# Kernel tuning notes

Measured on AMD Instinct MI355X. Metric: run time of the kernel, lower is better.

Reference implementation:

```python
import jax, jax.numpy as jnp
import numpy as np

B, I, H = 8192, 1024, 1024


def _linear_params(key, out_dim, in_dim):
    kw, kb = jax.random.split(key)
    bound = 1.0 / np.sqrt(in_dim)
    w = jax.random.uniform(kw, (out_dim, in_dim), jnp.float32, -bound, bound)
    b = jax.random.uniform(kb, (out_dim,), jnp.float32, -bound, bound)
    return w, b


def setup_inputs() -> dict:
    key = jax.random.key(0)
    ks = jax.random.split(key, 11)
    x = jax.random.normal(ks[0], (B, I), jnp.float32)
    h = jax.random.normal(ks[1], (B, H), jnp.float32)
    c = jax.random.normal(ks[2], (B, H), jnp.float32)
    # 4 gates: forget(f), input-mask(i), input-candidate(g, tanh), output(o)
    wf_i, bf_i = _linear_params(ks[3], H, I)
    wf_h, bf_h = _linear_params(ks[4], H, H)
    wi_i, bi_i = _linear_params(ks[5], H, I)
    wi_h, bi_h = _linear_params(ks[6], H, H)
    wg_i, bg_i = _linear_params(ks[7], H, I)
    wg_h, bg_h = _linear_params(ks[8], H, H)
    wo_i, bo_i = _linear_params(ks[9], H, I)
    wo_h, bo_h = _linear_params(ks[10], H, H)
    return dict(x=x, h=h, c=c,
                wf_i=wf_i, bf_i=bf_i, wf_h=wf_h, bf_h=bf_h,
                wi_i=wi_i, bi_i=bi_i, wi_h=wi_h, bi_h=bi_h,
                wg_i=wg_i, bg_i=bg_i, wg_h=wg_h, bg_h=bg_h,
                wo_i=wo_i, bo_i=bo_i, wo_h=wo_h, bo_h=bo_h)


def _gate(x, h, w_i, b_i, w_h, b_h, nonlin):
    # Linear(x) + Linear(h) then nonlinearity, matching torch nn.Linear (x @ W.T + b)
    pre = jnp.dot(x, w_i.T) + b_i + jnp.dot(h, w_h.T) + b_h
    return nonlin(pre)


def reference(x, h, c,
              wf_i, bf_i, wf_h, bf_h,
              wi_i, bi_i, wi_h, bi_h,
              wg_i, bg_i, wg_h, bg_h,
              wo_i, bo_i, wo_h, bo_h):
    ft = _gate(x, h, wf_i, bf_i, wf_h, bf_h, jax.nn.sigmoid)
    it = _gate(x, h, wi_i, bi_i, wi_h, bi_h, jax.nn.sigmoid)
    gt = _gate(x, h, wg_i, bg_i, wg_h, bg_h, jnp.tanh)
    ct = ft * c + it * gt
    ot = _gate(x, h, wo_i, bo_i, wo_h, bo_h, jax.nn.sigmoid)
    ht = ot * jnp.tanh(ct)
    return (ht, ct)
```

## Files before the change

kernel.cpp:

```cpp
#include <hip/hip_runtime.h>
#include <hip/hip_bf16.h>

typedef __hip_bfloat16 bf16;
typedef __attribute__((ext_vector_type(8))) short bf16x8;
typedef __attribute__((ext_vector_type(4))) float f32x4;

#define AS1 __attribute__((address_space(1)))
#define AS3 __attribute__((address_space(3)))

__device__ __forceinline__ void async16(const void* g, void* l) {
  __builtin_amdgcn_global_load_lds((const AS1 void*)g, (AS3 void*)l, 16, 0, 0);
}

__device__ __forceinline__ float fsigmoid(float x) { return 1.0f / (1.0f + __expf(-x)); }
__device__ __forceinline__ float ftanh(float x)    { return 1.0f - 2.0f / (__expf(2.0f * x) + 1.0f); }

__device__ __forceinline__ bf16x8 pack8(float4 lo, float4 hi) {
  union { bf16x8 v; unsigned int u[4]; } r;
  r.u[0] = (__float_as_uint(lo.y) & 0xFFFF0000u) | (__float_as_uint(lo.x) >> 16);
  r.u[1] = (__float_as_uint(lo.w) & 0xFFFF0000u) | (__float_as_uint(lo.z) >> 16);
  r.u[2] = (__float_as_uint(hi.y) & 0xFFFF0000u) | (__float_as_uint(hi.x) >> 16);
  r.u[3] = (__float_as_uint(hi.w) & 0xFFFF0000u) | (__float_as_uint(hi.z) >> 16);
  return r.v;
}

__global__ __launch_bounds__(256) void prep_bf16(
    const float* __restrict__ x, const float* __restrict__ h,
    const float* __restrict__ wfi, const float* __restrict__ wii,
    const float* __restrict__ wgi, const float* __restrict__ woi,
    const float* __restrict__ wfh, const float* __restrict__ wih,
    const float* __restrict__ wgh, const float* __restrict__ woh,
    bf16* __restrict__ dst)
{
  const int NC = 3 * 1024 * 1024;
  for (int ci = blockIdx.x * 256 + threadIdx.x; ci < NC; ci += gridDim.x * 256) {
    const float* src; size_t soff, doff;
    if (ci < (1 << 20)) {
      int m = ci >> 7, k = (ci & 127) << 3;
      src = x; soff = (size_t)m * 1024 + k; doff = (size_t)m * 2048 + k;
    } else if (ci < (2 << 20)) {
      int c2 = ci - (1 << 20);
      int m = c2 >> 7, k = (c2 & 127) << 3;
      src = h; soff = (size_t)m * 1024 + k; doff = (size_t)m * 2048 + 1024 + k;
    } else {
      int we  = ci - (2 << 20);
      int mat = we >> 17;
      int wl  = we & ((1 << 17) - 1);
      int hh  = wl >> 7, k = (wl & 127) << 3;
      int g   = mat & 3;
      src = (mat == 0) ? wfi : (mat == 1) ? wii : (mat == 2) ? wgi : (mat == 3) ? woi
          : (mat == 4) ? wfh : (mat == 5) ? wih : (mat == 6) ? wgh : woh;
      soff = (size_t)hh * 1024 + k;
      doff = (size_t)8192 * 2048
           + (size_t)(((hh >> 6) << 8) + (g << 6) + (hh & 63)) * 2048
           + ((mat >> 2) << 10) + k;
    }
    float4 lo = *(const float4*)(src + soff);
    float4 hi = *(const float4*)(src + soff + 4);
    *(bf16x8*)(dst + doff) = pack8(lo, hi);
  }
}

#define VMCNT(N) do { asm volatile("s_waitcnt vmcnt(" #N ")" ::: "memory"); \
                      __builtin_amdgcn_sched_barrier(0); } while (0)

#define PH(t_, kh_, mh_, STAGE_STMT, VMW)                                     \
  {                                                                           \
    const char* Ab = smem + (((t_) & 1) << 16) + ((kh_) << 14);               \
    const char* Bb = Ab + 32768;                                              \
    if ((mh_) == 0) {                                                         \
      _Pragma("unroll") for (int n = 0; n < 4; ++n)                           \
        bfr[n] = *(const bf16x8*)(Bb + boff + (n << 10));                     \
    }                                                                         \
    bf16x8 afr[4];                                                            \
    _Pragma("unroll") for (int i = 0; i < 4; ++i)                             \
      afr[i] = *(const bf16x8*)(Ab + aoff + ((((mh_) << 2) + i) << 10));      \
    STAGE_STMT;                                                               \
    __builtin_amdgcn_s_barrier();                                             \
    __builtin_amdgcn_s_setprio(1);                                            \
    _Pragma("unroll") for (int i = 0; i < 4; ++i)                             \
      _Pragma("unroll") for (int n = 0; n < 4; ++n)                           \
        acc[((mh_) << 2) + i][n] = __builtin_amdgcn_mfma_f32_16x16x32_bf16(   \
            afr[i], bfr[n], acc[((mh_) << 2) + i][n], 0, 0, 0);               \
    __builtin_amdgcn_s_setprio(0);                                            \
    VMW;                                                                      \
    __builtin_amdgcn_s_barrier();                                             \
  }

__global__ __launch_bounds__(512, 2) void lstm_mfma(
    const bf16* __restrict__ ws,
    const float* __restrict__ c,
    const float* __restrict__ bfi, const float* __restrict__ bfh,
    const float* __restrict__ bii, const float* __restrict__ bih,
    const float* __restrict__ bgi, const float* __restrict__ bgh,
    const float* __restrict__ boi, const float* __restrict__ boh,
    float* __restrict__ out)
{
  __shared__ __align__(16) char smem[135168];

  const int tid  = threadIdx.x;
  const int lane = tid & 63;
  const int w    = tid >> 6;
  const int wr   = w >> 2;
  const int wc   = w & 3;
  const int l15  = lane & 15;
  const int quad = lane >> 4;

  const int orig = blockIdx.x;
  const int xcd  = orig & 7;
  const int li   = orig >> 3;
  const int by   = ((xcd >> 1) << 3) + (li & 7);
  const int bx   = ((xcd & 1) << 3) + (li >> 3);
  const int bg0  = by << 8;

  const bf16* Ag = ws + (size_t)bg0 * 2048;
  const bf16* Bg = ws + (size_t)8192 * 2048 + (size_t)(bx << 8) * 2048;

  const int r2 = lane >> 2;
  const int sl = lane & 3;
  const int schunk = ((sl ^ ((r2 >> 1) & 3)) << 3);

  const int slotA = ((quad ^ ((l15 >> 1) & 3)) << 4);
  const int aoff  = ((wr << 7) + l15) * 64 + slotA;
  const int boff  = ((wc << 6) + l15) * 64 + slotA;

  f32x4 acc[8][4];
#pragma unroll
  for (int i = 0; i < 8; ++i)
#pragma unroll
    for (int j = 0; j < 4; ++j) acc[i][j] = (f32x4){0.f, 0.f, 0.f, 0.f};

  auto stageA = [&](int t_, int kh_) {
    const bf16* s = Ag + (size_t)(t_ << 6) + (kh_ << 5) + schunk;
    char* d = smem + ((t_ & 1) << 16) + (kh_ << 14) + (w << 10);
#pragma unroll
    for (int r = 0; r < 2; ++r)
      async16(s + ((size_t)((((r << 3) + w) << 4) + r2)) * 2048, d + (r << 13));
  };
  auto stageB = [&](int t_, int kh_) {
    const bf16* s = Bg + (size_t)(t_ << 6) + (kh_ << 5) + schunk;
    char* d = smem + ((t_ & 1) << 16) + 32768 + (kh_ << 14) + (w << 10);
#pragma unroll
    for (int r = 0; r < 2; ++r)
      async16(s + ((size_t)((((r << 3) + w) << 4) + r2)) * 2048, d + (r << 13));
  };

  stageA(0, 0); stageB(0, 0); stageA(0, 1); stageB(0, 1); stageA(1, 0); stageB(1, 0);
  VMCNT(8);
  __builtin_amdgcn_s_barrier();

  for (int t = 0; t < 30; ++t) {
    bf16x8 bfr[4];
    PH(t, 0, 0, { stageA(t + 1, 1); }, )
    PH(t, 0, 1, { stageB(t + 1, 1); }, VMCNT(8))
    PH(t, 1, 0, { stageA(t + 2, 0); }, )
    PH(t, 1, 1, { stageB(t + 2, 0); }, VMCNT(8))
  }
  {
    const int t = 30;
    bf16x8 bfr[4];
    PH(t, 0, 0, { stageA(31, 1); }, )
    PH(t, 0, 1, { stageB(31, 1); }, VMCNT(8))
    PH(t, 1, 0, , )
    PH(t, 1, 1, , VMCNT(4))
  }
  {
    const int t = 31;
    bf16x8 bfr[4];
    PH(t, 0, 0, , )
    PH(t, 0, 1, , VMCNT(0))
    PH(t, 1, 0, , )
    PH(t, 1, 1, , )
  }

  float* Act = (float*)smem;
  const float* bI = (wc == 0) ? bfi : (wc == 1) ? bii : (wc == 2) ? bgi : boi;
  const float* bH = (wc == 0) ? bfh : (wc == 1) ? bih : (wc == 2) ? bgh : boh;
  const int hcol0 = bx << 6;
  float biasv[4];
#pragma unroll
  for (int n = 0; n < 4; ++n)
    biasv[n] = bI[hcol0 + n * 16 + l15] + bH[hcol0 + n * 16 + l15];

  const size_t outCT = (size_t)8192 * 1024;
  const bool istanh = (wc == 2);

#pragma unroll
  for (int p = 0; p < 2; ++p) {
    __syncthreads();
    if (wr == p) {
      float* Aw = Act + wc * 8448;
#pragma unroll
      for (int m = 0; m < 8; ++m)
#pragma unroll
        for (int n = 0; n < 4; ++n)
#pragma unroll
          for (int r = 0; r < 4; ++r) {
            const float v = acc[m][n][r] + biasv[n];
            Aw[(m * 16 + quad * 4 + r) * 66 + n * 16 + l15] = istanh ? ftanh(v) : fsigmoid(v);
          }
    }
    __syncthreads();
#pragma unroll
    for (int it = 0; it < 16; ++it) {
      const int idx = it * 512 + tid;
      const int row = idx >> 6, col = idx & 63;
      const float fv = Act[row * 66 + col];
      const float iv = Act[8448 + row * 66 + col];
      const float gv = Act[16896 + row * 66 + col];
      const float ov = Act[25344 + row * 66 + col];
      const size_t gi = (size_t)(bg0 + p * 128 + row) * 1024 + hcol0 + col;
      const float ctv = fv * c[gi] + iv * gv;
      const float htv = ov * ftanh(ctv);
      out[gi]         = htv;
      out[outCT + gi] = ctv;
    }
  }
}

__global__ __launch_bounds__(256) void lstm_fused(
    const float* __restrict__ x, const float* __restrict__ h, const float* __restrict__ c,
    const float* __restrict__ wfi, const float* __restrict__ bfi, const float* __restrict__ wfh, const float* __restrict__ bfh,
    const float* __restrict__ wii, const float* __restrict__ bii, const float* __restrict__ wih, const float* __restrict__ bih,
    const float* __restrict__ wgi, const float* __restrict__ bgi, const float* __restrict__ wgh, const float* __restrict__ bgh,
    const float* __restrict__ woi, const float* __restrict__ boi, const float* __restrict__ woh, const float* __restrict__ boh,
    float* __restrict__ out)
{
  __shared__ __align__(16) char smem[33792];
  short* As = (short*)smem;
  short* Bs = As + 8192;
  float* Epi = (float*)smem;

  const int tid  = threadIdx.x;
  const int lane = tid & 63;
  const int w    = tid >> 6;
  const int l15  = lane & 15;
  const int quad = lane >> 4;
  const int rq   = w >> 1;
  const int cq   = w & 1;
  const int rowoff = lane >> 3;
  const int ch   = lane & 7;
  const int dstch = ch ^ rowoff;

  const int bg0 = blockIdx.y << 7;
  const int hb  = blockIdx.x << 5;

  const float* WgI = (w == 0) ? wfi : (w == 1) ? wii : (w == 2) ? wgi : woi;
  const float* WgH = (w == 0) ? wfh : (w == 1) ? wih : (w == 2) ? wgh : woh;

  size_t aoff[4], boff2[4];
#pragma unroll
  for (int q = 0; q < 4; ++q) {
    const int u = (w << 2) + q;
    aoff[q]  = (size_t)((u << 3) + rowoff) * 1024 + (ch << 3);
    boff2[q] = (size_t)((q << 3) + rowoff) * 1024 + (ch << 3);
  }

  f32x4 acc[4][4];
#pragma unroll
  for (int i = 0; i < 4; ++i)
#pragma unroll
    for (int j = 0; j < 4; ++j) acc[i][j] = (f32x4){0.f, 0.f, 0.f, 0.f};

  const int arow = (rq * 64 + l15) * 64;
  const int brow = (cq * 64 + l15) * 64;
  const int sw   = l15 & 7;
  const int c0   = ((0 + quad) ^ sw) << 3;
  const int c1   = ((4 + quad) ^ sw) << 3;

  float4 A0[4], A1[4], B0[4], B1[4];
  auto issue = [&](int KT) {
    const float* Ab = ((KT < 16) ? x : h)     + (size_t)bg0 * 1024 + ((KT & 15) << 6);
    const float* Bb = ((KT < 16) ? WgI : WgH) + (size_t)hb  * 1024 + ((KT & 15) << 6);
#pragma unroll
    for (int q = 0; q < 4; ++q) {
      const float* pa = Ab + aoff[q];
      const float* pb = Bb + boff2[q];
      A0[q] = *(const float4*)pa; A1[q] = *(const float4*)(pa + 4);
      B0[q] = *(const float4*)pb; B1[q] = *(const float4*)(pb + 4);
    }
  };

  issue(0);
  for (int kt = 0; kt < 32; ++kt) {
    __syncthreads();
#pragma unroll
    for (int q = 0; q < 4; ++q) {
      const int u = (w << 2) + q;
      *(bf16x8*)(As + (u * 8 + rowoff) * 64 + (dstch << 3)) = pack8(A0[q], A1[q]);
      *(bf16x8*)(Bs + (u * 8 + rowoff) * 64 + (dstch << 3)) = pack8(B0[q], B1[q]);
    }
    __syncthreads();
    if (kt < 31) issue(kt + 1);

#pragma unroll
    for (int s = 0; s < 2; ++s) {
      const int cs = s ? c1 : c0;
      bf16x8 a[4], b[4];
#pragma unroll
      for (int i = 0; i < 4; ++i) a[i] = *(const bf16x8*)(As + arow + i * 1024 + cs);
#pragma unroll
      for (int j = 0; j < 4; ++j) b[j] = *(const bf16x8*)(Bs + brow + j * 1024 + cs);
#pragma unroll
      for (int i = 0; i < 4; ++i)
#pragma unroll
        for (int j = 0; j < 4; ++j)
          acc[i][j] = __builtin_amdgcn_mfma_f32_16x16x32_bf16(a[i], b[j], acc[i][j], 0, 0, 0);
    }
  }

  const float* bAi = cq ? bgi : bfi;
  const float* bAh = cq ? bgh : bfh;
  const float* bBi = cq ? boi : bii;
  const float* bBh = cq ? boh : bih;
  float biasv[4];
  biasv[0] = bAi[hb + l15]      + bAh[hb + l15];
  biasv[1] = bAi[hb + 16 + l15] + bAh[hb + 16 + l15];
  biasv[2] = bBi[hb + l15]      + bBh[hb + l15];
  biasv[3] = bBi[hb + 16 + l15] + bBh[hb + 16 + l15];

  const size_t outCT = (size_t)8192 * 1024;

#pragma unroll
  for (int p = 0; p < 2; ++p) {
    __syncthreads();
    if (rq == p) {
#pragma unroll
      for (int j = 0; j < 4; ++j) {
        const int  n  = cq * 64 + j * 16 + l15;
        const bool ut = (cq == 1) && (j < 2);
        const float bj = biasv[j];
#pragma unroll
        for (int i = 0; i < 4; ++i)
#pragma unroll
          for (int r = 0; r < 4; ++r) {
            const float v = acc[i][j][r] + bj;
            Epi[(i * 16 + quad * 4 + r) * 132 + n] = ut ? ftanh(v) : fsigmoid(v);
          }
      }
    }
    __syncthreads();
#pragma unroll
    for (int it = 0; it < 8; ++it) {
      const int pair = it * 256 + tid;
      const int row  = pair >> 5;
      const int hl   = pair & 31;
      const float fv = Epi[row * 132 + hl];
      const float iv = Epi[row * 132 + 32 + hl];
      const float gv = Epi[row * 132 + 64 + hl];
      const float ov = Epi[row * 132 + 96 + hl];
      const size_t idx = (size_t)(bg0 + p * 64 + row) * 1024 + hb + hl;
      const float ctv = fv * c[idx] + iv * gv;
      const float htv = ov * ftanh(ctv);
      out[idx]         = htv;
      out[outCT + idx] = ctv;
    }
  }
}

extern "C" void kernel_launch(void* const* d_in, const int* in_sizes, int n_in,
                              void* d_out, int out_size, void* d_ws, size_t ws_size,
                              hipStream_t stream) {
  const float* p[19];
  for (int i = 0; i < 19; ++i) p[i] = (const float*)d_in[i];
  const size_t need = (size_t)24 * 1024 * 1024 * sizeof(bf16);
  if (ws_size >= need) {
    prep_bf16<<<dim3(2048), dim3(256), 0, stream>>>(
        p[0], p[1],
        p[3], p[7], p[11], p[15],
        p[5], p[9], p[13], p[17],
        (bf16*)d_ws);
    lstm_mfma<<<dim3(512), dim3(512), 0, stream>>>(
        (const bf16*)d_ws, p[2],
        p[4], p[6], p[8], p[10], p[12], p[14], p[16], p[18],
        (float*)d_out);
  } else {
    lstm_fused<<<dim3(32, 64), dim3(256), 0, stream>>>(
        p[0], p[1], p[2],
        p[3], p[4], p[5], p[6],
        p[7], p[8], p[9], p[10],
        p[11], p[12], p[13], p[14],
        p[15], p[16], p[17], p[18],
        (float*)d_out);
  }
}
```

Baseline: 349.9 us.

## Software-pipeline LDS fragment reads one phase ahead of MFMA compute

```diff
diff --git a/kernel.cpp b/kernel.cpp
--- a/kernel.cpp
+++ b/kernel.cpp
@@ -64,28 +64,28 @@
 #define VMCNT(N) do { asm volatile("s_waitcnt vmcnt(" #N ")" ::: "memory"); \
                       __builtin_amdgcn_sched_barrier(0); } while (0)
 
-#define PH(t_, kh_, mh_, STAGE_STMT, VMW)                                     \
-  {                                                                           \
-    const char* Ab = smem + (((t_) & 1) << 16) + ((kh_) << 14);               \
-    const char* Bb = Ab + 32768;                                              \
-    if ((mh_) == 0) {                                                         \
-      _Pragma("unroll") for (int n = 0; n < 4; ++n)                           \
-        bfr[n] = *(const bf16x8*)(Bb + boff + (n << 10));                     \
-    }                                                                         \
-    bf16x8 afr[4];                                                            \
-    _Pragma("unroll") for (int i = 0; i < 4; ++i)                             \
-      afr[i] = *(const bf16x8*)(Ab + aoff + ((((mh_) << 2) + i) << 10));      \
-    STAGE_STMT;                                                               \
-    __builtin_amdgcn_s_barrier();                                             \
+#define BAR __builtin_amdgcn_s_barrier()
+
+#define RD_A(dst, t_, kh_, mh_) do {                                          \
+    const char* Ab_ = smem + (((t_) & 1) << 16) + ((kh_) << 14);              \
+    _Pragma("unroll") for (int i_ = 0; i_ < 4; ++i_)                          \
+      dst[i_] = *(const bf16x8*)(Ab_ + aoff + ((((mh_) << 2) + i_) << 10));   \
+  } while (0)
+
+#define RD_B(dst, t_, kh_) do {                                               \
+    const char* Bb_ = smem + (((t_) & 1) << 16) + ((kh_) << 14) + 32768;      \
+    _Pragma("unroll") for (int n_ = 0; n_ < 4; ++n_)                          \
+      dst[n_] = *(const bf16x8*)(Bb_ + boff + (n_ << 10));                    \
+  } while (0)
+
+#define MM(a_, b_, mh_) do {                                                  \
     __builtin_amdgcn_s_setprio(1);                                            \
-    _Pragma("unroll") for (int i = 0; i < 4; ++i)                             \
-      _Pragma("unroll") for (int n = 0; n < 4; ++n)                           \
-        acc[((mh_) << 2) + i][n] = __builtin_amdgcn_mfma_f32_16x16x32_bf16(   \
-            afr[i], bfr[n], acc[((mh_) << 2) + i][n], 0, 0, 0);               \
+    _Pragma("unroll") for (int i_ = 0; i_ < 4; ++i_)                          \
+      _Pragma("unroll") for (int n_ = 0; n_ < 4; ++n_)                        \
+        acc[((mh_) << 2) + i_][n_] = __builtin_amdgcn_mfma_f32_16x16x32_bf16( \
+            a_[i_], b_[n_], acc[((mh_) << 2) + i_][n_], 0, 0, 0);             \
     __builtin_amdgcn_s_setprio(0);                                            \
-    VMW;                                                                      \
-    __builtin_amdgcn_s_barrier();                                             \
-  }
+  } while (0)
 
 __global__ __launch_bounds__(512, 2) void lstm_mfma(
     const bf16* __restrict__ ws,
@@ -145,32 +145,41 @@
       async16(s + ((size_t)((((r << 3) + w) << 4) + r2)) * 2048, d + (r << 13));
   };
 
+  bf16x8 A0[4], A1[4], B0[4], B1[4];
+
   stageA(0, 0); stageB(0, 0); stageA(0, 1); stageB(0, 1); stageA(1, 0); stageB(1, 0);
   VMCNT(8);
-  __builtin_amdgcn_s_barrier();
+  BAR;
+  RD_A(A0, 0, 0, 0); RD_B(B0, 0, 0);
 
   for (int t = 0; t < 30; ++t) {
-    bf16x8 bfr[4];
-    PH(t, 0, 0, { stageA(t + 1, 1); }, )
-    PH(t, 0, 1, { stageB(t + 1, 1); }, VMCNT(8))
-    PH(t, 1, 0, { stageA(t + 2, 0); }, )
-    PH(t, 1, 1, { stageB(t + 2, 0); }, VMCNT(8))
+    RD_A(A1, t, 0, 1); stageA(t + 1, 1);
+    BAR; MM(A0, B0, 0); VMCNT(6); BAR;
+    RD_A(A0, t, 1, 0); RD_B(B1, t, 1); stageB(t + 1, 1);
+    BAR; MM(A1, B0, 1); BAR;
+    RD_A(A1, t, 1, 1); stageA(t + 2, 0);
+    BAR; MM(A0, B1, 0); VMCNT(6); BAR;
+    RD_A(A0, t + 1, 0, 0); RD_B(B0, t + 1, 0); stageB(t + 2, 0);
+    BAR; MM(A1, B1, 1); BAR;
   }
   {
-    const int t = 30;
-    bf16x8 bfr[4];
-    PH(t, 0, 0, { stageA(31, 1); }, )
-    PH(t, 0, 1, { stageB(31, 1); }, VMCNT(8))
-    PH(t, 1, 0, , )
-    PH(t, 1, 1, , VMCNT(4))
+    RD_A(A1, 30, 0, 1); stageA(31, 1);
+    BAR; MM(A0, B0, 0); VMCNT(6); BAR;
+    RD_A(A0, 30, 1, 0); RD_B(B1, 30, 1); stageB(31, 1);
+    BAR; MM(A1, B0, 1); BAR;
+    RD_A(A1, 30, 1, 1);
+    BAR; MM(A0, B1, 0); VMCNT(4); BAR;
+    RD_A(A0, 31, 0, 0); RD_B(B0, 31, 0);
+    BAR; MM(A1, B1, 1); BAR;
   }
   {
-    const int t = 31;
-    bf16x8 bfr[4];
-    PH(t, 0, 0, , )
-    PH(t, 0, 1, , VMCNT(0))
-    PH(t, 1, 0, , )
-    PH(t, 1, 1, , )
+    RD_A(A1, 31, 0, 1);
+    BAR; MM(A0, B0, 0); VMCNT(0); BAR;
+    RD_A(A0, 31, 1, 0); RD_B(B1, 31, 1);
+    BAR; MM(A1, B0, 1); BAR;
+    RD_A(A1, 31, 1, 1);
+    BAR; MM(A0, B1, 0); BAR;
+    MM(A1, B1, 1);
   }
 
   float* Act = (float*)smem;
```

Result: slower. 357.6 us (+2.2%).

## Merge GEMM main loop into two phases per k-tile with one-tile prefetch

Applied to the files above, without the earlier changes.

```diff
diff --git a/kernel.cpp b/kernel.cpp
--- a/kernel.cpp
+++ b/kernel.cpp
@@ -64,27 +64,27 @@
 #define VMCNT(N) do { asm volatile("s_waitcnt vmcnt(" #N ")" ::: "memory"); \
                       __builtin_amdgcn_sched_barrier(0); } while (0)
 
-#define PH(t_, kh_, mh_, STAGE_STMT, VMW)                                     \
+#define BAR __builtin_amdgcn_s_barrier()
+
+#define PHASE(t_, kh_, STAGE_STMT, VMW)                                       \
   {                                                                           \
-    const char* Ab = smem + (((t_) & 1) << 16) + ((kh_) << 14);               \
-    const char* Bb = Ab + 32768;                                              \
-    if ((mh_) == 0) {                                                         \
-      _Pragma("unroll") for (int n = 0; n < 4; ++n)                           \
-        bfr[n] = *(const bf16x8*)(Bb + boff + (n << 10));                     \
-    }                                                                         \
-    bf16x8 afr[4];                                                            \
-    _Pragma("unroll") for (int i = 0; i < 4; ++i)                             \
-      afr[i] = *(const bf16x8*)(Ab + aoff + ((((mh_) << 2) + i) << 10));      \
+    const char* Ab_ = smem + (((t_) & 1) << 16) + ((kh_) << 14);              \
+    const char* Bb_ = Ab_ + 32768;                                            \
+    bf16x8 af[8], bf[4];                                                      \
+    _Pragma("unroll") for (int i_ = 0; i_ < 8; ++i_)                          \
+      af[i_] = *(const bf16x8*)(Ab_ + aoff + (i_ << 10));                     \
+    _Pragma("unroll") for (int n_ = 0; n_ < 4; ++n_)                          \
+      bf[n_] = *(const bf16x8*)(Bb_ + boff + (n_ << 10));                     \
     STAGE_STMT;                                                               \
-    __builtin_amdgcn_s_barrier();                                             \
+    BAR;                                                                      \
     __builtin_amdgcn_s_setprio(1);                                            \
-    _Pragma("unroll") for (int i = 0; i < 4; ++i)                             \
-      _Pragma("unroll") for (int n = 0; n < 4; ++n)                           \
-        acc[((mh_) << 2) + i][n] = __builtin_amdgcn_mfma_f32_16x16x32_bf16(   \
-            afr[i], bfr[n], acc[((mh_) << 2) + i][n], 0, 0, 0);               \
+    _Pragma("unroll") for (int i_ = 0; i_ < 8; ++i_)                          \
+      _Pragma("unroll") for (int n_ = 0; n_ < 4; ++n_)                        \
+        acc[i_][n_] = __builtin_amdgcn_mfma_f32_16x16x32_bf16(                \
+            af[i_], bf[n_], acc[i_][n_], 0, 0, 0);                            \
     __builtin_amdgcn_s_setprio(0);                                            \
     VMW;                                                                      \
-    __builtin_amdgcn_s_barrier();                                             \
+    BAR;                                                                      \
   }
 
 __global__ __launch_bounds__(512, 2) void lstm_mfma(
@@ -145,32 +145,17 @@
       async16(s + ((size_t)((((r << 3) + w) << 4) + r2)) * 2048, d + (r << 13));
   };
 
-  stageA(0, 0); stageB(0, 0); stageA(0, 1); stageB(0, 1); stageA(1, 0); stageB(1, 0);
-  VMCNT(8);
-  __builtin_amdgcn_s_barrier();
-
-  for (int t = 0; t < 30; ++t) {
-    bf16x8 bfr[4];
-    PH(t, 0, 0, { stageA(t + 1, 1); }, )
-    PH(t, 0, 1, { stageB(t + 1, 1); }, VMCNT(8))
-    PH(t, 1, 0, { stageA(t + 2, 0); }, )
-    PH(t, 1, 1, { stageB(t + 2, 0); }, VMCNT(8))
+  stageA(0, 0); stageB(0, 0); stageA(0, 1); stageB(0, 1);
+  VMCNT(4);
+  BAR;
+
+  for (int t = 0; t < 31; ++t) {
+    PHASE(t, 0, { stageA(t + 1, 0); stageB(t + 1, 0); }, VMCNT(4))
+    PHASE(t, 1, { stageA(t + 1, 1); stageB(t + 1, 1); }, VMCNT(4))
   }
   {
-    const int t = 30;
-    bf16x8 bfr[4];
-    PH(t, 0, 0, { stageA(31, 1); }, )
-    PH(t, 0, 1, { stageB(31, 1); }, VMCNT(8))
-    PH(t, 1, 0, , )
-    PH(t, 1, 1, , VMCNT(4))
-  }
-  {
-    const int t = 31;
-    bf16x8 bfr[4];
-    PH(t, 0, 0, , )
-    PH(t, 0, 1, , VMCNT(0))
-    PH(t, 1, 0, , )
-    PH(t, 1, 1, , )
+    PHASE(31, 0, , VMCNT(0))
+    PHASE(31, 1, , )
   }
 
   float* Act = (float*)smem;
```

New measurement: 358.4 us. 1.02x slower.
